# Optimization experiments

Measured on AMD Instinct MI355X. Metric: run time of the kernel, lower is better.

## Reference

```python
import jax, jax.numpy as jnp
import numpy as np

GROUP_SIZE = 128

def setup_inputs() -> dict:
    key = jax.random.key(0)
    k0, k1, k2, k3 = jax.random.split(key, 4)
    B, S, K, N = 4, 16, 8192, 28672
    G = GROUP_SIZE
    x = jax.random.normal(k0, (B, S, K), dtype=jnp.float16)
    # packed uint8 stored as int32 (2 int4 nibbles per byte along K)
    w_packed = jax.random.randint(k1, (K // 2, N), 0, 256, dtype=jnp.int32)
    # per-group positive scales, typical magnitude for int4 quant of fp16 weights
    scales = (jax.random.uniform(k2, (K // G, N), dtype=jnp.float32) * 0.02 + 1e-4).astype(jnp.float16)
    bias = (jax.random.normal(k3, (N,), dtype=jnp.float16) * 0.02).astype(jnp.float16)
    return {"x": x, "w_packed": w_packed, "scales": scales, "bias": bias}

def _dequant(w_packed, scales):
    # w_packed: [K//2, N] ints in [0,256); low nibble -> even k, high nibble -> odd k
    low = (w_packed & 15) - 8          # [K//2, N] int32 in [-8, 7]
    high = ((w_packed >> 4) & 15) - 8  # [K//2, N]
    Kh, N = w_packed.shape
    w_int = jnp.stack([low, high], axis=1).reshape(Kh * 2, N)  # interleave -> [K, N]
    s = jnp.repeat(scales, GROUP_SIZE, axis=0)                 # [K, N] fp16
    return w_int.astype(jnp.float16) * s                       # [K, N] fp16

def reference(x, w_packed, scales, bias):
    # x: [B, S, K] fp16 -> y: [B, S, N] fp16
    w = _dequant(w_packed, scales)                 # [K, N] fp16
    lead = x.shape[:-1]
    x2 = x.reshape(-1, x.shape[-1])                # [M, K]
    # fp32 accumulation, fp16 output (matches Triton kernel's tl.dot accumulator)
    y = jnp.dot(x2, w, preferred_element_type=jnp.float32).astype(jnp.float16)
    y = y + bias
    return y.reshape(*lead, -1)
```

## Files before the change

### kernel.cpp

```cpp
#include <hip/hip_runtime.h>


typedef short  short8  __attribute__((ext_vector_type(8)));
typedef float  float4v __attribute__((ext_vector_type(4)));
typedef int    int4v   __attribute__((ext_vector_type(4)));
typedef unsigned int uint4v __attribute__((ext_vector_type(4)));

constexpr int Kd = 8192;
constexpr int Nd = 28672;
constexpr int KSPLIT = 4;
constexpr int GPS = 16;
constexpr int LDS_STRIDE = 68;

__device__ __forceinline__ unsigned f32_to_bf16_rn(float f) {
    unsigned u = __builtin_bit_cast(unsigned, f);
    return (u + 0x7FFFu + ((u >> 16) & 1u)) >> 16;
}

__device__ __forceinline__ void sync_lds() {
    asm volatile("s_waitcnt lgkmcnt(0)\n\ts_barrier" ::: "memory");
}

__global__ __launch_bounds__(256)
void init_y_kernel(const float* __restrict__ bias, float* __restrict__ y) {
    const int gid = blockIdx.x * 256 + threadIdx.x;
    const int m  = gid / (Nd / 4);
    const int nq = gid % (Nd / 4);
    ((float4v*)y)[(long)m * (Nd / 4) + nq] = ((const float4v*)bias)[nq];
}

__global__ __launch_bounds__(256)
void cvt_x_kernel(const float* __restrict__ x, unsigned short* __restrict__ o) {
    const int i = (blockIdx.x * 256 + threadIdx.x) * 8;
    float4v a = *(const float4v*)(x + i);
    float4v b = *(const float4v*)(x + i + 4);
    union { unsigned short s[8]; short8 v; } r;
    #pragma unroll
    for (int j = 0; j < 4; ++j) {
        r.s[j]     = (unsigned short)f32_to_bf16_rn(a[j]);
        r.s[4 + j] = (unsigned short)f32_to_bf16_rn(b[j]);
    }
    *(short8*)(o + i) = r.v;
}

__global__ __launch_bounds__(256, 4)
void int4_main_kernel(const unsigned short* __restrict__ xb,
                      const int*            __restrict__ wp,
                      const float*          __restrict__ scales,
                      float*                __restrict__ y)
{
    __shared__ unsigned lds_w[2 * 64 * LDS_STRIDE];

    const int t    = threadIdx.x;
    const int lane = t & 63;
    const int wv   = t >> 6;
    const int q    = lane >> 4;
    const int c    = lane & 15;
    const int n0   = blockIdx.x * 64;
    const int kz   = blockIdx.y;

    const int sr = t >> 4, ss = t & 15;
    const int*   wp_b = wp + (long)(kz * 1024 + sr) * Nd + n0 + 4 * ss;
    const float* sc_b = scales + (long)(kz * GPS) * Nd + n0 + 4 * ss;
    const unsigned short* xb_b = xb + (long)c * Kd + kz * 2048 + q * 8;

    float4v acc[4] = {};
    int4v wc[4], wn[4];
    float4v scur, snxt;

    #pragma unroll
    for (int i = 0; i < 4; ++i)
        wc[i] = *(const int4v*)(wp_b + (long)i * 16 * Nd);
    scur = *(const float4v*)(sc_b);

    for (int g = 0; g < GPS; ++g) {
        unsigned* buf = &lds_w[(g & 1) * (64 * LDS_STRIDE)];

        const unsigned short* xg = xb_b + g * 128;
        short8 areg[16];
        #pragma unroll
        for (int it = 0; it < 4; ++it)
            #pragma unroll
            for (int mt = 0; mt < 4; ++mt)
                areg[it * 4 + mt] = *(const short8*)(xg + it * 32 + (long)mt * 16 * Kd);

        if (g + 1 < GPS) {
            const int* wg = wp_b + (long)(g + 1) * 64 * Nd;
            #pragma unroll
            for (int i = 0; i < 4; ++i)
                wn[i] = *(const int4v*)(wg + (long)i * 16 * Nd);
            snxt = *(const float4v*)(sc_b + (long)(g + 1) * Nd);
        }

        #pragma unroll
        for (int i = 0; i < 4; ++i) {
            uint4v pk;
            #pragma unroll
            for (int j = 0; j < 4; ++j) {
                float lo = (float)((wc[i][j] & 15) - 8) * scur[j];
                float hi = (float)(((wc[i][j] >> 4) & 15) - 8) * scur[j];
                pk[j] = f32_to_bf16_rn(lo) | (f32_to_bf16_rn(hi) << 16);
            }
            *(uint4v*)&buf[(i * 16 + sr) * LDS_STRIDE + 4 * ss] = pk;
        }

        sync_lds();

        #pragma unroll
        for (int it = 0; it < 4; ++it) {
            union { short8 h; unsigned u[4]; } bu;
            #pragma unroll
            for (int i = 0; i < 4; ++i)
                bu.u[i] = buf[(it * 16 + q * 4 + i) * LDS_STRIDE + wv * 16 + c];
            const short8 b = bu.h;
            #pragma unroll
            for (int mt = 0; mt < 4; ++mt)
                acc[mt] = __builtin_amdgcn_mfma_f32_16x16x32_bf16(
                              areg[it * 4 + mt], b, acc[mt], 0, 0, 0);
        }

        #pragma unroll
        for (int i = 0; i < 4; ++i) wc[i] = wn[i];
        scur = snxt;
    }

    const int nw = n0 + wv * 16 + c;
    #pragma unroll
    for (int mt = 0; mt < 4; ++mt)
        #pragma unroll
        for (int r = 0; r < 4; ++r)
            atomicAdd(&y[(long)(mt * 16 + q * 4 + r) * Nd + nw], acc[mt][r]);
}

__global__ __launch_bounds__(256, 6)
void int4_main_nows_kernel(const float* __restrict__ xf,
                           const int*   __restrict__ wp,
                           const float* __restrict__ scales,
                           float*       __restrict__ y)
{
    __shared__ unsigned lds_w[64 * LDS_STRIDE];
    const int t = threadIdx.x, lane = t & 63, wv = t >> 6;
    const int q = lane >> 4, c = lane & 15;
    const int n0 = blockIdx.x * 64, kz = blockIdx.y;
    const int sr = t >> 4, ss = t & 15;
    const int*   wp_b = wp + (long)(kz * 1024 + sr) * Nd + n0 + 4 * ss;
    const float* sc_b = scales + (long)(kz * GPS) * Nd + n0 + 4 * ss;
    const float* xf_b = xf + (long)c * Kd + kz * 2048 + q * 8;
    float4v acc[4] = {};

    for (int g = 0; g < GPS; ++g) {
        const float4v s4 = *(const float4v*)(sc_b + (long)g * Nd);
        const int* wg = wp_b + (long)g * 64 * Nd;
        #pragma unroll
        for (int i = 0; i < 4; ++i) {
            int4v v = *(const int4v*)(wg + (long)i * 16 * Nd);
            uint4v pk;
            #pragma unroll
            for (int j = 0; j < 4; ++j) {
                float lo = (float)((v[j] & 15) - 8) * s4[j];
                float hi = (float)(((v[j] >> 4) & 15) - 8) * s4[j];
                pk[j] = f32_to_bf16_rn(lo) | (f32_to_bf16_rn(hi) << 16);
            }
            *(uint4v*)&lds_w[(i * 16 + sr) * LDS_STRIDE + 4 * ss] = pk;
        }
        __syncthreads();
        const float* xg = xf_b + g * 128;
        #pragma unroll
        for (int it = 0; it < 4; ++it) {
            union { short8 h; unsigned u[4]; } bu;
            #pragma unroll
            for (int i = 0; i < 4; ++i)
                bu.u[i] = lds_w[(it * 16 + q * 4 + i) * LDS_STRIDE + wv * 16 + c];
            const short8 b = bu.h;
            const float* xk = xg + it * 32;
            #pragma unroll
            for (int mt = 0; mt < 4; ++mt) {
                float4v a0 = *(const float4v*)(xk + (long)mt * 16 * Kd);
                float4v a1 = *(const float4v*)(xk + (long)mt * 16 * Kd + 4);
                union { unsigned short s[8]; short8 v; } r;
                #pragma unroll
                for (int j = 0; j < 4; ++j) {
                    r.s[j]     = (unsigned short)f32_to_bf16_rn(a0[j]);
                    r.s[4 + j] = (unsigned short)f32_to_bf16_rn(a1[j]);
                }
                acc[mt] = __builtin_amdgcn_mfma_f32_16x16x32_bf16(r.v, b, acc[mt], 0, 0, 0);
            }
        }
        __syncthreads();
    }
    const int nw = n0 + wv * 16 + c;
    #pragma unroll
    for (int mt = 0; mt < 4; ++mt)
        #pragma unroll
        for (int r = 0; r < 4; ++r)
            atomicAdd(&y[(long)(mt * 16 + q * 4 + r) * Nd + nw], acc[mt][r]);
}

extern "C" void kernel_launch(void* const* d_in, const int* in_sizes, int n_in,
                              void* d_out, int out_size, void* d_ws, size_t ws_size,
                              hipStream_t stream) {
    const float* x      = (const float*)d_in[0];
    const int*   wp     = (const int*)d_in[1];
    const float* scales = (const float*)d_in[2];
    const float* bias   = (const float*)d_in[3];
    float*       y      = (float*)d_out;

    init_y_kernel<<<dim3(1792), dim3(256), 0, stream>>>(bias, y);

    const size_t xb_bytes = (size_t)64 * Kd * sizeof(unsigned short);
    dim3 grid(Nd / 64, KSPLIT);
    dim3 block(256);

    if (ws_size >= xb_bytes) {
        unsigned short* xb = (unsigned short*)d_ws;
        cvt_x_kernel<<<dim3(256), dim3(256), 0, stream>>>(x, xb);
        int4_main_kernel<<<grid, block, 0, stream>>>(xb, wp, scales, y);
    } else {
        int4_main_nows_kernel<<<grid, block, 0, stream>>>(x, wp, scales, y);
    }
}
```

Baseline: 755.1 us.

## Stream packed weights into LDS asynchronously and dequantize after the LDS read

The main kernel now copies the raw packed int4 words straight from global memory into a double-buffered LDS tile with global_load_lds, instead of holding them in registers, dequantizing, and then storing bf16 to LDS. Dequantization moves to the consumer side: each lane dequantizes the words it reads from LDS, using an FMA with one per-column scale. The goal is to drop the register staging and the VGPR-to-LDS store path, and to keep the next group's weight fetch in flight while MFMAs run. In exchange it adds a second barrier per group, relies on hand-placed vmcnt waits for correctness, and removes the LDS row padding, so the LDS reads may hit bank conflicts.

New measurement: 720.5 us. 4.6% less time.

```diff
diff --git a/kernel.cpp b/kernel.cpp
--- a/kernel.cpp
+++ b/kernel.cpp
@@ -10,15 +10,17 @@
 constexpr int Nd = 28672;
 constexpr int KSPLIT = 4;
 constexpr int GPS = 16;
-constexpr int LDS_STRIDE = 68;
 
 __device__ __forceinline__ unsigned f32_to_bf16_rn(float f) {
     unsigned u = __builtin_bit_cast(unsigned, f);
     return (u + 0x7FFFu + ((u >> 16) & 1u)) >> 16;
 }
 
-__device__ __forceinline__ void sync_lds() {
-    asm volatile("s_waitcnt lgkmcnt(0)\n\ts_barrier" ::: "memory");
+__device__ __forceinline__ void async_copy16(const int* g, unsigned* l) {
+    __builtin_amdgcn_global_load_lds(
+        (const __attribute__((address_space(1))) unsigned int*)g,
+        (__attribute__((address_space(3))) unsigned int*)l,
+        16, 0, 0);
 }
 
 __global__ __launch_bounds__(256)
@@ -49,7 +51,7 @@
                       const float*          __restrict__ scales,
                       float*                __restrict__ y)
 {
-    __shared__ unsigned lds_w[2 * 64 * LDS_STRIDE];
+    __shared__ unsigned lds_w[2 * 4096];
 
     const int t    = threadIdx.x;
     const int lane = t & 63;
@@ -59,69 +61,58 @@
     const int n0   = blockIdx.x * 64;
     const int kz   = blockIdx.y;
 
-    const int sr = t >> 4, ss = t & 15;
-    const int*   wp_b = wp + (long)(kz * 1024 + sr) * Nd + n0 + 4 * ss;
-    const float* sc_b = scales + (long)(kz * GPS) * Nd + n0 + 4 * ss;
+    const int* wbase = wp + (long)(kz * 1024 + wv * 16 + (lane >> 4)) * Nd
+                          + n0 + 4 * (lane & 15);
+    const int lbase = wv * 16 * 64;
+
     const unsigned short* xb_b = xb + (long)c * Kd + kz * 2048 + q * 8;
+    const float* sc_b = scales + (long)(kz * GPS) * Nd + n0 + wv * 16 + c;
 
     float4v acc[4] = {};
-    int4v wc[4], wn[4];
-    float4v scur, snxt;
 
     #pragma unroll
     for (int i = 0; i < 4; ++i)
-        wc[i] = *(const int4v*)(wp_b + (long)i * 16 * Nd);
-    scur = *(const float4v*)(sc_b);
+        async_copy16(wbase + (long)i * 4 * Nd, &lds_w[lbase + i * 256]);
 
     for (int g = 0; g < GPS; ++g) {
-        unsigned* buf = &lds_w[(g & 1) * (64 * LDS_STRIDE)];
-
+        short8 areg[16];
         const unsigned short* xg = xb_b + g * 128;
-        short8 areg[16];
         #pragma unroll
         for (int it = 0; it < 4; ++it)
             #pragma unroll
             for (int mt = 0; mt < 4; ++mt)
                 areg[it * 4 + mt] = *(const short8*)(xg + it * 32 + (long)mt * 16 * Kd);
+        const float s   = sc_b[(long)g * Nd];
+        const float m8s = -8.0f * s;
 
         if (g + 1 < GPS) {
-            const int* wg = wp_b + (long)(g + 1) * 64 * Nd;
+            const int* wg = wbase + (long)(g + 1) * 64 * Nd;
+            unsigned* lb = &lds_w[((g + 1) & 1) * 4096 + lbase];
             #pragma unroll
             for (int i = 0; i < 4; ++i)
-                wn[i] = *(const int4v*)(wg + (long)i * 16 * Nd);
-            snxt = *(const float4v*)(sc_b + (long)(g + 1) * Nd);
-        }
-
-        #pragma unroll
-        for (int i = 0; i < 4; ++i) {
-            uint4v pk;
-            #pragma unroll
-            for (int j = 0; j < 4; ++j) {
-                float lo = (float)((wc[i][j] & 15) - 8) * scur[j];
-                float hi = (float)(((wc[i][j] >> 4) & 15) - 8) * scur[j];
-                pk[j] = f32_to_bf16_rn(lo) | (f32_to_bf16_rn(hi) << 16);
-            }
-            *(uint4v*)&buf[(i * 16 + sr) * LDS_STRIDE + 4 * ss] = pk;
-        }
-
-        sync_lds();
-
+                async_copy16(wg + (long)i * 4 * Nd, lb + i * 256);
+        }
+
+        asm volatile("s_waitcnt vmcnt(4)\n\ts_barrier" ::: "memory");
+
+        const unsigned* buf = &lds_w[(g & 1) * 4096];
         #pragma unroll
         for (int it = 0; it < 4; ++it) {
             union { short8 h; unsigned u[4]; } bu;
             #pragma unroll
-            for (int i = 0; i < 4; ++i)
-                bu.u[i] = buf[(it * 16 + q * 4 + i) * LDS_STRIDE + wv * 16 + c];
-            const short8 b = bu.h;
+            for (int i = 0; i < 4; ++i) {
+                unsigned v = buf[(it * 16 + q * 4 + i) * 64 + wv * 16 + c];
+                float lo = fmaf((float)(v & 15u), s, m8s);
+                float hi = fmaf((float)((v >> 4) & 15u), s, m8s);
+                bu.u[i] = f32_to_bf16_rn(lo) | (f32_to_bf16_rn(hi) << 16);
+            }
             #pragma unroll
             for (int mt = 0; mt < 4; ++mt)
                 acc[mt] = __builtin_amdgcn_mfma_f32_16x16x32_bf16(
-                              areg[it * 4 + mt], b, acc[mt], 0, 0, 0);
-        }
-
-        #pragma unroll
-        for (int i = 0; i < 4; ++i) wc[i] = wn[i];
-        scur = snxt;
+                              areg[it * 4 + mt], bu.h, acc[mt], 0, 0, 0);
+        }
+
+        asm volatile("s_waitcnt lgkmcnt(0)\n\ts_barrier" ::: "memory");
     }
 
     const int nw = n0 + wv * 16 + c;
@@ -138,6 +129,7 @@
                            const float* __restrict__ scales,
                            float*       __restrict__ y)
 {
+    constexpr int LDS_STRIDE = 68;
     __shared__ unsigned lds_w[64 * LDS_STRIDE];
     const int t = threadIdx.x, lane = t & 63, wv = t >> 6;
     const int q = lane >> 4, c = lane & 15;
```
